# Performance work log

Hardware: AMD Instinct MI355X
Metric: run time of the kernel (lower is better)

## Reference

```python
import jax, jax.numpy as jnp
import numpy as np

EPS = 1e-5  # torch LayerNorm default


def setup_inputs() -> dict:
    key = jax.random.key(0)
    ks = jax.random.split(key, 6)
    B, C, H, W, D = 8, 128, 64, 64, 32
    x = jax.random.normal(ks[0], (B, C, H, W), dtype=jnp.float32)
    gamma = jnp.ones((C,), dtype=jnp.float32)
    beta = jnp.zeros((C,), dtype=jnp.float32)
    Wq = jax.random.normal(ks[1], (D, C), dtype=jnp.float32) * 0.02
    Wk = jax.random.normal(ks[2], (D, C), dtype=jnp.float32) * 0.02
    Wv = jax.random.normal(ks[3], (C, C), dtype=jnp.float32) * 0.02
    Wo = jax.random.normal(ks[4], (C, C), dtype=jnp.float32) * (1.0 / np.sqrt(C))
    bo = jnp.zeros((C,), dtype=jnp.float32)
    return {"x": x, "gamma": gamma, "beta": beta, "Wq": Wq, "Wk": Wk,
            "Wv": Wv, "Wo": Wo, "bo": bo}


def reference(x, gamma, beta, Wq, Wk, Wv, Wo, bo):
    B, C, H, W = x.shape
    # LayerNorm over channel dim (applied in NHWC in the original)
    xn = x.transpose(0, 2, 3, 1)                       # [B,H,W,C]
    mu = xn.mean(-1, keepdims=True)
    var = ((xn - mu) ** 2).mean(-1, keepdims=True)
    xn = (xn - mu) * jax.lax.rsqrt(var + EPS) * gamma + beta
    xn = xn.transpose(0, 3, 1, 2)                      # [B,C,H,W]
    # 1x1-conv projections == channel matmuls
    q = jnp.einsum('dc,bchw->bdhw', Wq, xn)
    k = jnp.einsum('dc,bchw->bdhw', Wk, xn)
    v = jnp.einsum('oc,bchw->bohw', Wv, xn)
    # full spatial attention: scores [B,H,W,H,W], softmax over key positions
    scores = jnp.einsum('bchw,bcxy->bhwxy', q, k)
    scores = scores.reshape(B, H, W, H * W)
    attn = jax.nn.softmax(scores, axis=-1).reshape(B, H, W, H, W)
    out = jnp.einsum('bhwxy,bcxy->bchw', attn, v)
    out = jnp.einsum('oc,bchw->bohw', Wo, out) + bo[None, :, None, None]
    return out + x
```

## Files before the change

kernel.cpp:

```cpp
#include <hip/hip_runtime.h>


#define NB 8
#define CCH 128
#define NTOK 4096
#define DQK 32
#define KT 64
#define PARTSZ 4194304

typedef __attribute__((ext_vector_type(8))) short bf16x8;
typedef __attribute__((ext_vector_type(4))) float f32x4;
typedef unsigned short u16;
typedef unsigned int u32;

static __device__ __forceinline__ f32x4 mfma16(bf16x8 a, bf16x8 b, f32x4 c) {
  return __builtin_amdgcn_mfma_f32_16x16x32_bf16(a, b, c, 0, 0, 0);
}
static __device__ __forceinline__ u16 f2bf(float f) {
  union { float f; u32 u; } cv; cv.f = f;
  u32 u = cv.u;
  u += 0x7fffu + ((u >> 16) & 1u);
  return (u16)(u >> 16);
}
static __device__ __forceinline__ float bf2f(u16 v) {
  union { u32 u; float f; } cv; cv.u = ((u32)v) << 16;
  return cv.f;
}
static __device__ __forceinline__ u32 cvtpk(float lo, float hi) {
  u32 d;
  asm("v_cvt_pk_bf16_f32 %0, %1, %2" : "=v"(d) : "v"(lo), "v"(hi));
  return d;
}
static __device__ __forceinline__ void gload16(const void* g, void* l) {
  __builtin_amdgcn_global_load_lds(
      (const __attribute__((address_space(1))) void*)g,
      (__attribute__((address_space(3))) void*)l, 16, 0, 0);
}

__global__ __launch_bounds__(256) void wconv_kernel(
    const float* __restrict__ Wq, const float* __restrict__ Wk,
    const float* __restrict__ Wv, const float* __restrict__ Wo,
    u16* __restrict__ wcomb) {
  int idx = blockIdx.x * 256 + threadIdx.x;
  int r = idx >> 7;
  float v;
  if (r < 32)        v = Wq[idx];
  else if (r < 64)   v = Wk[idx - 4096];
  else if (r < 192)  v = Wv[idx - 8192];
  else               v = Wo[idx - 24576];
  wcomb[idx] = f2bf(v);
}

__global__ __launch_bounds__(256) void lnqkv_kernel(
    const float* __restrict__ x, const float* __restrict__ gamma,
    const float* __restrict__ beta, const u16* __restrict__ wcomb,
    u16* __restrict__ Qg, u16* __restrict__ Kg, u16* __restrict__ Vt) {
  __shared__ float tile[128][64];
  __shared__ float red[2][4][64];
  __shared__ u16   xt[64][130];
  int t = threadIdx.x;
  int lane = t & 63, cq = t >> 6;
  int b = blockIdx.x >> 6;
  int posb = (blockIdx.x & 63) << 6;
  const float* xb = x + ((size_t)b * CCH) * NTOK + posb;
  for (int i = 0; i < 32; ++i) {
    int c = cq * 32 + i;
    tile[c][lane] = xb[(size_t)c * NTOK + lane];
  }
  __syncthreads();
  float s = 0.f, s2 = 0.f;
  for (int i = 0; i < 32; ++i) {
    float v = tile[cq * 32 + i][lane];
    s += v; s2 += v * v;
  }
  red[0][cq][lane] = s; red[1][cq][lane] = s2;
  __syncthreads();
  float mu  = (red[0][0][lane] + red[0][1][lane] + red[0][2][lane] + red[0][3][lane]) * (1.f / 128.f);
  float ex2 = (red[1][0][lane] + red[1][1][lane] + red[1][2][lane] + red[1][3][lane]) * (1.f / 128.f);
  float rstd = rsqrtf(ex2 - mu * mu + 1e-5f);
  for (int i = 0; i < 32; ++i) {
    int c = cq * 32 + i;
    float v = (tile[c][lane] - mu) * rstd * gamma[c] + beta[c];
    xt[lane][c] = f2bf(v);
  }
  __syncthreads();
  int w = t >> 6, row16 = lane & 15, kgrp = lane >> 4;
  bf16x8 af[4];
  for (int ks = 0; ks < 4; ++ks)
    af[ks] = *(const bf16x8*)&xt[w * 16 + row16][ks * 32 + kgrp * 8];
  f32x4 zero = {0.f, 0.f, 0.f, 0.f};
  f32x4 acc[12];
  for (int nt = 0; nt < 12; ++nt) {
    acc[nt] = zero;
    for (int ks = 0; ks < 4; ++ks) {
      bf16x8 bf = *(const bf16x8*)&wcomb[(size_t)(nt * 16 + row16) * CCH + ks * 32 + kgrp * 8];
      acc[nt] = mfma16(af[ks], bf, acc[nt]);
    }
  }
  int tok0 = b * NTOK + posb;
  for (int nt = 0; nt < 12; ++nt) {
    int col = nt * 16 + row16;
    for (int r = 0; r < 4; ++r) {
      int token = tok0 + w * 16 + kgrp * 4 + r;
      if (col < 32) {
        Qg[(size_t)token * DQK + col] = f2bf(acc[nt][r] * 1.44269504f);
      } else if (col < 64) {
        Kg[(size_t)token * DQK + (col - 32)] = f2bf(acc[nt][r]);
      } else {
        int tl = token & (NTOK - 1);
        int kp = (tl & ~31) | ((tl & 12) << 1) | ((tl & 16) >> 2) | (tl & 3);
        Vt[((size_t)b * CCH + (col - 64)) * NTOK + kp] = f2bf(acc[nt][r]);
      }
    }
  }
}

template <int NS>
__global__ __launch_bounds__(256, 4) void attn_kernel(
    const u16* __restrict__ Qg, const u16* __restrict__ Kg,
    const u16* __restrict__ Vt, u16* __restrict__ Op,
    float* __restrict__ lp) {
  __shared__ u16 lds[2][10240];
  constexpr int KSEG = NTOK / NS;
  constexpr int NTILE = KSEG / KT;
  constexpr int BSH = (NS == 4) ? 7 : 6;
  int t = threadIdx.x;
  int w = t >> 6, lane = t & 63;
  int row16 = lane & 15, kgrp = lane >> 4;

  int cpx = (256 * NS) >> 3;
  int logical = (blockIdx.x & 7) * cpx + (blockIdx.x >> 3);
  int qblk = logical & 31;
  int part = (logical >> 5) & (NS - 1);
  int b = logical >> BSH;
  int q0 = qblk * 128;
  int kt0 = part * KSEG;

  const u16* Qb = Qg + ((size_t)(b * NTOK + q0 + w * 32)) * DQK;
  bf16x8 qf0 = *(const bf16x8*)&Qb[(size_t)row16 * DQK + kgrp * 8];
  bf16x8 qf1 = *(const bf16x8*)&Qb[(size_t)(16 + row16) * DQK + kgrp * 8];

  bf16x8 ones_b;
  {
    short val = (row16 == 0) ? (short)0x3F80 : (short)0;
    for (int j = 0; j < 8; ++j) ones_b[j] = val;
  }

  int korig = (lane & 7) ^ (lane >> 3);
  int kconst = (((lane >> 3) * 2 + (korig >> 2)) * 32) + (korig & 3) * 8;
  const u16* ksrc = Kg + (size_t)(b * NTOK + kt0) * DQK + kconst;
  int cV = t >> 3;
  int sV = (t & 7) ^ (cV & 7);
  const u16* vsrc = Vt + ((size_t)b * CCH + cV) * NTOK + kt0 + sV * 8;
  int vdst = w * 512;

  f32x4 zero = {0.f, 0.f, 0.f, 0.f};
  f32x4 o0[8], o1[8], ol0, ol1;
#pragma unroll
  for (int i = 0; i < 8; ++i) { o0[i] = zero; o1[i] = zero; }
  ol0 = zero; ol1 = zero;

  auto stage = [&](int bi, int tile) {
    const u16* kp_ = ksrc + (size_t)tile * (KT * DQK);
#pragma unroll
    for (int ii = 0; ii < 4; ++ii)
      gload16(kp_ + ii * 512, &lds[bi][ii * 512]);
    const u16* vp_ = vsrc + tile * KT;
    gload16(vp_,          &lds[bi][2048 + vdst]);
    gload16(vp_ + 131072, &lds[bi][2048 + 2048 + vdst]);
    gload16(vp_ + 262144, &lds[bi][2048 + 4096 + vdst]);
    gload16(vp_ + 393216, &lds[bi][2048 + 6144 + vdst]);
  };

  auto loadK = [&](int bi, bf16x8* kf) {
#pragma unroll
    for (int nt = 0; nt < 4; ++nt) {
      int slot = (nt * 8 + (row16 >> 1)) * 8 +
                 ((((row16 & 1) << 2) + kgrp) ^ (row16 >> 1));
      kf[nt] = *(const bf16x8*)&lds[bi][slot * 8];
    }
  };

  auto compute = [&](int bi, const bf16x8* kf) {
    const u16* vb = &lds[bi][2048];
    f32x4 sa0[4], sa1[4];
#pragma unroll
    for (int nt = 0; nt < 4; ++nt) {
      sa0[nt] = mfma16(kf[nt], qf0, zero);
      sa1[nt] = mfma16(kf[nt], qf1, zero);
    }
#pragma unroll
    for (int nt = 0; nt < 4; ++nt)
      for (int r = 0; r < 4; ++r) {
        sa0[nt][r] = __builtin_amdgcn_exp2f(sa0[nt][r]);
        sa1[nt][r] = __builtin_amdgcn_exp2f(sa1[nt][r]);
      }
    union PU { u32 d[4]; bf16x8 v; };
    PU pf0[2], pf1[2];
#pragma unroll
    for (int ks = 0; ks < 2; ++ks) {
      pf0[ks].d[0] = cvtpk(sa0[2 * ks][0], sa0[2 * ks][1]);
      pf0[ks].d[1] = cvtpk(sa0[2 * ks][2], sa0[2 * ks][3]);
      pf0[ks].d[2] = cvtpk(sa0[2 * ks + 1][0], sa0[2 * ks + 1][1]);
      pf0[ks].d[3] = cvtpk(sa0[2 * ks + 1][2], sa0[2 * ks + 1][3]);
      pf1[ks].d[0] = cvtpk(sa1[2 * ks][0], sa1[2 * ks][1]);
      pf1[ks].d[1] = cvtpk(sa1[2 * ks][2], sa1[2 * ks][3]);
      pf1[ks].d[2] = cvtpk(sa1[2 * ks + 1][0], sa1[2 * ks + 1][1]);
      pf1[ks].d[3] = cvtpk(sa1[2 * ks + 1][2], sa1[2 * ks + 1][3]);
    }
    __builtin_amdgcn_s_setprio(1);
    ol0 = mfma16(pf0[0].v, ones_b, ol0);
    ol0 = mfma16(pf0[1].v, ones_b, ol0);
    ol1 = mfma16(pf1[0].v, ones_b, ol1);
    ol1 = mfma16(pf1[1].v, ones_b, ol1);
#pragma unroll
    for (int ks = 0; ks < 2; ++ks)
#pragma unroll
      for (int ntc = 0; ntc < 8; ++ntc) {
        int vslot = (ntc * 16 + row16) * 8 + (((ks << 2) + kgrp) ^ (row16 & 7));
        bf16x8 vf = *(const bf16x8*)&vb[vslot * 8];
        o0[ntc] = mfma16(pf0[ks].v, vf, o0[ntc]);
        o1[ntc] = mfma16(pf1[ks].v, vf, o1[ntc]);
      }
    __builtin_amdgcn_s_setprio(0);
  };

  bf16x8 kf[4];
  stage(0, 0);
  asm volatile("s_waitcnt vmcnt(0)" ::: "memory");
  loadK(0, kf);
  __builtin_amdgcn_s_barrier();
  int cur = 0;
  for (int tile = 0; tile < NTILE - 1; ++tile) {
    stage(cur ^ 1, tile + 1);
    compute(cur, kf);
    asm volatile("s_waitcnt vmcnt(0)" ::: "memory");
    loadK(cur ^ 1, kf);
    __builtin_amdgcn_s_barrier();
    cur ^= 1;
  }
  compute(cur, kf);

  u32 word[32];
#pragma unroll
  for (int sub = 0; sub < 2; ++sub) {
#pragma unroll
    for (int ntc = 0; ntc < 8; ++ntc) {
      f32x4 ov = sub ? o1[ntc] : o0[ntc];
      word[sub * 16 + ntc * 2]     = cvtpk(ov[0], ov[1]);
      word[sub * 16 + ntc * 2 + 1] = cvtpk(ov[2], ov[3]);
    }
  }
  u16* Opw = Op + (size_t)part * PARTSZ;
  size_t blkb = ((size_t)(b * NTOK + q0)) * CCH;
#pragma unroll
  for (int j = 0; j < 8; ++j) {
    uint4 v4;
    v4.x = word[4 * j]; v4.y = word[4 * j + 1];
    v4.z = word[4 * j + 2]; v4.w = word[4 * j + 3];
    *(uint4*)&Opw[blkb + w * 4096 + j * 512 + lane * 8] = v4;
  }
  int tokb = b * NTOK + q0 + w * 32;
  if (row16 == 0) {
#pragma unroll
    for (int r = 0; r < 4; ++r) {
      lp[part * 32768 + tokb + kgrp * 4 + r] = ol0[r];
      lp[part * 32768 + tokb + 16 + kgrp * 4 + r] = ol1[r];
    }
  }
}

__global__ __launch_bounds__(256) void out_kernel(
    const u16* __restrict__ Op, const float* __restrict__ lp, int ns,
    const u16* __restrict__ wcomb, const float* __restrict__ bo,
    const float* __restrict__ x, float* __restrict__ out) {
  __shared__ float lred[128];
  __shared__ u16 xt[128][132];
  int t = threadIdx.x;
  int w = t >> 6, lane = t & 63;
  int row16 = lane & 15, kgrp = lane >> 4;
  int blk = blockIdx.x;
  int tok0 = blk * 128;
  int b = tok0 >> 12, tloc = tok0 & (NTOK - 1);

  if (t < 128) {
    float s = 0.f;
    for (int p = 0; p < ns; ++p) s += lp[p * 32768 + tok0 + t];
    lred[t] = 1.f / s;
  }
  __syncthreads();
  float linv[2][4];
#pragma unroll
  for (int sub = 0; sub < 2; ++sub)
#pragma unroll
    for (int r = 0; r < 4; ++r)
      linv[sub][r] = lred[w * 32 + sub * 16 + kgrp * 4 + r];

  size_t blkb = (size_t)tok0 * CCH;
#pragma unroll
  for (int j = 0; j < 8; ++j) {
    float s[8] = {0.f, 0.f, 0.f, 0.f, 0.f, 0.f, 0.f, 0.f};
    for (int p = 0; p < ns; ++p) {
      uint4 v4 = *(const uint4*)&Op[(size_t)p * PARTSZ + blkb + w * 4096 + j * 512 + lane * 8];
      u32 ww[4] = {v4.x, v4.y, v4.z, v4.w};
#pragma unroll
      for (int m = 0; m < 4; ++m) {
        s[2 * m]     += bf2f((u16)(ww[m] & 0xffffu));
        s[2 * m + 1] += bf2f((u16)(ww[m] >> 16));
      }
    }
    int sub = j >> 2;
#pragma unroll
    for (int m = 0; m < 4; ++m) {
      int i = 4 * j + m;
      int ntc = (i >> 1) & 7, pr = i & 1;
      int c = ntc * 16 + row16;
#pragma unroll
      for (int dd = 0; dd < 2; ++dd) {
        int r = 2 * pr + dd;
        xt[w * 32 + sub * 16 + kgrp * 4 + r][c] = f2bf(s[2 * m + dd] * linv[sub][r]);
      }
    }
  }
  __syncthreads();

  f32x4 zero = {0.f, 0.f, 0.f, 0.f};
  f32x4 acc[2][8];
#pragma unroll
  for (int sub = 0; sub < 2; ++sub)
    for (int nt = 0; nt < 8; ++nt) acc[sub][nt] = zero;
#pragma unroll
  for (int ks = 0; ks < 4; ++ks) {
    bf16x8 af0 = *(const bf16x8*)&xt[w * 32 + row16][ks * 32 + kgrp * 8];
    bf16x8 af1 = *(const bf16x8*)&xt[w * 32 + 16 + row16][ks * 32 + kgrp * 8];
#pragma unroll
    for (int nt = 0; nt < 8; ++nt) {
      bf16x8 bfv = *(const bf16x8*)&wcomb[(size_t)(192 + nt * 16 + row16) * CCH + ks * 32 + kgrp * 8];
      acc[0][nt] = mfma16(af0, bfv, acc[0][nt]);
      acc[1][nt] = mfma16(af1, bfv, acc[1][nt]);
    }
  }
#pragma unroll
  for (int sub = 0; sub < 2; ++sub)
#pragma unroll
    for (int nt = 0; nt < 8; ++nt) {
      int cout = nt * 16 + row16;
      float bias = bo[cout];
      size_t base = ((size_t)b * CCH + cout) * NTOK + tloc + w * 32 + sub * 16 + kgrp * 4;
      float4 xr = *(const float4*)&x[base];
      float4 ov;
      ov.x = acc[sub][nt][0] + bias + xr.x;
      ov.y = acc[sub][nt][1] + bias + xr.y;
      ov.z = acc[sub][nt][2] + bias + xr.z;
      ov.w = acc[sub][nt][3] + bias + xr.w;
      *(float4*)&out[base] = ov;
    }
}

extern "C" void kernel_launch(void* const* d_in, const int* in_sizes, int n_in,
                              void* d_out, int out_size, void* d_ws, size_t ws_size,
                              hipStream_t stream) {
  const float* x     = (const float*)d_in[0];
  const float* gamma = (const float*)d_in[1];
  const float* beta  = (const float*)d_in[2];
  const float* Wq    = (const float*)d_in[3];
  const float* Wk    = (const float*)d_in[4];
  const float* Wv    = (const float*)d_in[5];
  const float* Wo    = (const float*)d_in[6];
  const float* bo    = (const float*)d_in[7];
  float* out = (float*)d_out;

  unsigned char* ws = (unsigned char*)d_ws;
  u16* Qg    = (u16*)(ws);
  u16* Kg    = (u16*)(ws + 2097152);
  u16* Vt    = (u16*)(ws + 4194304);
  u16* wcomb = (u16*)(ws + 12582912);
  float* lp  = (float*)(ws + 12664832);
  u16* Op    = (u16*)(ws + 13189120);

  int ns = (ws_size >= 46743552u) ? 4 : 2;

  wconv_kernel<<<160, 256, 0, stream>>>(Wq, Wk, Wv, Wo, wcomb);
  lnqkv_kernel<<<512, 256, 0, stream>>>(x, gamma, beta, wcomb, Qg, Kg, Vt);
  if (ns == 4)
    attn_kernel<4><<<1024, 256, 0, stream>>>(Qg, Kg, Vt, Op, lp);
  else
    attn_kernel<2><<<512, 256, 0, stream>>>(Qg, Kg, Vt, Op, lp);
  out_kernel<<<256, 256, 0, stream>>>(Op, lp, ns, wcomb, bo, x, out);
}
```

Measured before the change: 113.8 us.

## Coalesce V transpose stores via LDS and simplify K staging in attention

The projection kernel now stages the permuted V tile in shared memory and writes it to Vt with 16-byte vector stores instead of scattered 2-byte writes. In the attention kernel each thread issues a single K global-to-LDS load with its own swizzled address instead of four loads per thread. K fragments are now read from LDS inside compute rather than prefetched into registers before the barrier. This cuts uncoalesced global stores and load instruction count, at the cost of an extra barrier in the projection kernel and K LDS reads on the critical path of compute.

```diff
diff --git a/kernel.cpp b/kernel.cpp
--- a/kernel.cpp
+++ b/kernel.cpp
@@ -84,6 +84,7 @@
     xt[lane][c] = f2bf(v);
   }
   __syncthreads();
+  u16* vl = (u16*)tile;
   int w = t >> 6, row16 = lane & 15, kgrp = lane >> 4;
   bf16x8 af[4];
   for (int ks = 0; ks < 4; ++ks)
@@ -107,12 +108,19 @@
       } else if (col < 64) {
         Kg[(size_t)token * DQK + (col - 32)] = f2bf(acc[nt][r]);
       } else {
-        int tl = token & (NTOK - 1);
-        int kp = (tl & ~31) | ((tl & 12) << 1) | ((tl & 16) >> 2) | (tl & 3);
-        Vt[((size_t)b * CCH + (col - 64)) * NTOK + kp] = f2bf(acc[nt][r]);
-      }
-    }
-  }
+        int j = w * 16 + kgrp * 4 + r;
+        int kpl = (j & 32) | ((j & 12) << 1) | ((j & 16) >> 2) | (j & 3);
+        vl[(col - 64) * 72 + kpl] = f2bf(acc[nt][r]);
+      }
+    }
+  }
+  __syncthreads();
+  int c = t >> 1, hh = (t & 1) * 32;
+  u16* dst = Vt + ((size_t)b * CCH + c) * NTOK + posb + hh;
+  const u16* srcv = &vl[c * 72 + hh];
+#pragma unroll
+  for (int i = 0; i < 4; ++i)
+    *(uint4*)&dst[i * 8] = *(const uint4*)&srcv[i * 8];
 }
 
 template <int NS>
@@ -146,12 +154,16 @@
     for (int j = 0; j < 8; ++j) ones_b[j] = val;
   }
 
-  int korig = (lane & 7) ^ (lane >> 3);
-  int kconst = (((lane >> 3) * 2 + (korig >> 2)) * 32) + (korig & 3) * 8;
-  const u16* ksrc = Kg + (size_t)(b * NTOK + kt0) * DQK + kconst;
+  int pr = t >> 3, e8 = t & 7;
+  int korig = e8 ^ (pr & 7);
+  int kkey = pr * 2 + (korig >> 2);
+  int kfs = korig & 3;
+  const u16* ksrc = Kg + (size_t)(b * NTOK + kt0 + kkey) * DQK + kfs * 8;
   int cV = t >> 3;
-  int sV = (t & 7) ^ (cV & 7);
+  int sV = e8 ^ (cV & 7);
   const u16* vsrc = Vt + ((size_t)b * CCH + cV) * NTOK + kt0 + sV * 8;
+
+  int kdst = w * 512;
   int vdst = w * 512;
 
   f32x4 zero = {0.f, 0.f, 0.f, 0.f};
@@ -162,9 +174,7 @@
 
   auto stage = [&](int bi, int tile) {
     const u16* kp_ = ksrc + (size_t)tile * (KT * DQK);
-#pragma unroll
-    for (int ii = 0; ii < 4; ++ii)
-      gload16(kp_ + ii * 512, &lds[bi][ii * 512]);
+    gload16(kp_, &lds[bi][kdst]);
     const u16* vp_ = vsrc + tile * KT;
     gload16(vp_,          &lds[bi][2048 + vdst]);
     gload16(vp_ + 131072, &lds[bi][2048 + 2048 + vdst]);
@@ -172,22 +182,17 @@
     gload16(vp_ + 393216, &lds[bi][2048 + 6144 + vdst]);
   };
 
-  auto loadK = [&](int bi, bf16x8* kf) {
+  auto compute = [&](int bi) {
+    const u16* kb = &lds[bi][0];
+    const u16* vb = &lds[bi][2048];
+    f32x4 sa0[4], sa1[4];
 #pragma unroll
     for (int nt = 0; nt < 4; ++nt) {
       int slot = (nt * 8 + (row16 >> 1)) * 8 +
                  ((((row16 & 1) << 2) + kgrp) ^ (row16 >> 1));
-      kf[nt] = *(const bf16x8*)&lds[bi][slot * 8];
-    }
-  };
-
-  auto compute = [&](int bi, const bf16x8* kf) {
-    const u16* vb = &lds[bi][2048];
-    f32x4 sa0[4], sa1[4];
-#pragma unroll
-    for (int nt = 0; nt < 4; ++nt) {
-      sa0[nt] = mfma16(kf[nt], qf0, zero);
-      sa1[nt] = mfma16(kf[nt], qf1, zero);
+      bf16x8 kf = *(const bf16x8*)&kb[slot * 8];
+      sa0[nt] = mfma16(kf, qf0, zero);
+      sa1[nt] = mfma16(kf, qf1, zero);
     }
 #pragma unroll
     for (int nt = 0; nt < 4; ++nt)
@@ -225,21 +230,18 @@
     __builtin_amdgcn_s_setprio(0);
   };
 
-  bf16x8 kf[4];
   stage(0, 0);
   asm volatile("s_waitcnt vmcnt(0)" ::: "memory");
-  loadK(0, kf);
   __builtin_amdgcn_s_barrier();
   int cur = 0;
   for (int tile = 0; tile < NTILE - 1; ++tile) {
     stage(cur ^ 1, tile + 1);
-    compute(cur, kf);
+    compute(cur);
     asm volatile("s_waitcnt vmcnt(0)" ::: "memory");
-    loadK(cur ^ 1, kf);
     __builtin_amdgcn_s_barrier();
     cur ^= 1;
   }
-  compute(cur, kf);
+  compute(cur);
 
   u32 word[32];
 #pragma unroll
```

After: 115.9 us. Within noise of the previous version (+1.8%).
